# Performance work log

Measured on AMD Instinct MI355X. Metric: run time of the kernel, lower is better.

## Reference

```python
import jax, jax.numpy as jnp
import numpy as np

ALPHA = 1.0
K = 5          # kernel height == width
STRIDE = 1


def extract_patches(x, k, stride):
    """x: (N, C, H, W) -> (N, k*k*C, Ho, Wo), feature order (kh, kw, c)
    to match k.view(kh*kw*C, F) flattening of a (kh, kw, C, F) kernel."""
    p = jax.lax.conv_general_dilated_patches(x, (k, k), (stride, stride), 'VALID')
    N, _, Ho, Wo = p.shape
    C = x.shape[1]
    # conv_general_dilated_patches is channel-major: (C, kh, kw) -> reorder to (kh, kw, C)
    p = p.reshape(N, C, k, k, Ho, Wo).transpose(0, 2, 3, 1, 4, 5)
    return p.reshape(N, k * k * C, Ho, Wo)


def setup_inputs():
    key = jax.random.key(0)
    kx, kk1, kk2 = jax.random.split(key, 3)
    N, C, H, W = 8, 4, 64, 64
    F = 16
    # xavier-uniform-ish scale for kernels
    limit = float(np.sqrt(6.0 / (K * K * C + F)))
    x = jax.random.normal(kx, (N, C, H, W), jnp.float32)
    k1 = jax.random.uniform(kk1, (K, K, C, F), jnp.float32, -limit, limit)
    k2 = jax.random.uniform(kk2, (K, K, C, F), jnp.float32, -limit, limit)
    bias = jnp.zeros((F,), jnp.float32)
    return {"x": x, "k1": k1, "k2": k2, "bias": bias}


def _smooth_max(patches, kflat):
    # patches: (N, P, Ho, Wo); kflat: (P, F)
    z = patches[:, :, None] + kflat[None, :, :, None, None]  # (N, P, F, Ho, Wo)
    w = jax.nn.softmax(ALPHA * z, axis=1)  # exp(alpha*z)/sum over patch dim (stable)
    return jnp.sum(z * w, axis=1)          # (N, F, Ho, Wo)


def reference(x, k1, k2, bias):
    kh, kw, C, F = k1.shape
    patches = extract_patches(x, kh, STRIDE)        # (N, kh*kw*C, Ho, Wo)
    y11 = _smooth_max(patches, k1.reshape(-1, F))   # smooth-max of  x + k1
    y21 = _smooth_max(-patches, k2.reshape(-1, F))  # smooth-max of -x + k2
    return y11 + y21 + bias[None, :, None, None]
```

## Files before the change

kernel.cpp:

```cpp
#include <hip/hip_runtime.h>

#define NN 8
#define CC 4
#define HH 64
#define WW 64
#define KK 5
#define FF 16
#define HO 60
#define WO 60
#define PP (KK * KK * CC)


__global__ void smorph_weights(const float* __restrict__ k1,
                               const float* __restrict__ k2,
                               float4* __restrict__ wq) {
    int i = blockIdx.x * blockDim.x + threadIdx.x;
    if (i < PP * FF) {
        float a = k1[i], b = k2[i];
        float ea = __expf(a), eb = __expf(b);
        wq[i] = make_float4(ea, a * ea, eb, b * eb);
    }
}

__global__ __launch_bounds__(256) void smorph_conv(
        const float* __restrict__ x, const float4* __restrict__ wq,
        const float* __restrict__ bias, float* __restrict__ out) {
    __shared__ float4 pq[CC * KK * 64 + 4];

    int b = blockIdx.x;
    int n = b / HO;
    int ho = b % HO;
    int t = threadIdx.x;

    for (int i = t; i < CC * KK * 64; i += 256) {
        int w = i & 63;
        int cr = i >> 6;
        int c = cr / KK, r = cr - c * KK;
        float v = x[((n * CC + c) * HH + (ho + r)) * WW + w];
        float e1 = __expf(v), e2 = __expf(-v);
        pq[i] = make_float4(e1, v * e1, e2, -v * e2);
    }
    __syncthreads();

    int lane = t & 63;
    int fbase = __builtin_amdgcn_readfirstlane(t >> 6) * 4;

    float d1[4] = {0.f, 0.f, 0.f, 0.f}, n1[4] = {0.f, 0.f, 0.f, 0.f};
    float d2[4] = {0.f, 0.f, 0.f, 0.f}, n2[4] = {0.f, 0.f, 0.f, 0.f};

#pragma unroll 1
    for (int c = 0; c < CC; ++c) {
#pragma unroll
        for (int kh = 0; kh < KK; ++kh) {
            const float4* prow = &pq[(c * KK + kh) * 64 + lane];
#pragma unroll
            for (int kw = 0; kw < KK; ++kw) {
                float4 q = prow[kw];
                const float4* wp = wq + ((kh * KK + kw) * CC + c) * FF + fbase;
#pragma unroll
                for (int j = 0; j < 4; ++j) {
                    float4 ww = wp[j];
                    d1[j] = fmaf(q.x, ww.x, d1[j]);
                    n1[j] = fmaf(q.y, ww.x, n1[j]);
                    n1[j] = fmaf(q.x, ww.y, n1[j]);
                    d2[j] = fmaf(q.z, ww.z, d2[j]);
                    n2[j] = fmaf(q.w, ww.z, n2[j]);
                    n2[j] = fmaf(q.z, ww.w, n2[j]);
                }
            }
        }
    }

    if (lane < WO) {
#pragma unroll
        for (int j = 0; j < 4; ++j) {
            int f = fbase + j;
            out[((size_t)(n * FF + f) * HO + ho) * WO + lane] =
                n1[j] / d1[j] + n2[j] / d2[j] + bias[f];
        }
    }
}

extern "C" void kernel_launch(void* const* d_in, const int* in_sizes, int n_in,
                              void* d_out, int out_size, void* d_ws, size_t ws_size,
                              hipStream_t stream) {
    const float* x    = (const float*)d_in[0];
    const float* k1   = (const float*)d_in[1];
    const float* k2   = (const float*)d_in[2];
    const float* bias = (const float*)d_in[3];
    float* out = (float*)d_out;

    float4* wq = (float4*)d_ws;

    smorph_weights<<<(PP * FF + 255) / 256, 256, 0, stream>>>(k1, k2, wq);
    smorph_conv<<<480, 256, 0, stream>>>(x, wq, bias, out);
}
```

Measured before the change: 82.49 us.

## Fuse weight precompute into conv kernel, split channels across waves, pack FMAs

Removes the separate weight-exponentiation kernel and recomputes exp(k) weights per block into LDS, so the second launch and its dependency go away. The block grows to 512 threads, with two wave groups each covering half of the input channels, and a shared-memory reduction combines their partial sums. Accumulators use 2-wide float vectors so the compiler can emit packed FMAs. The cost is that every block redundantly recomputes 1600 weight exponentials, plus an extra barrier and LDS traffic for the reduction.

```diff
diff --git a/kernel.cpp b/kernel.cpp
--- a/kernel.cpp
+++ b/kernel.cpp
@@ -10,73 +10,97 @@
 #define WO 60
 #define PP (KK * KK * CC)
 
+typedef float v4f __attribute__((ext_vector_type(4)));
+typedef float v2f __attribute__((ext_vector_type(2)));
 
-__global__ void smorph_weights(const float* __restrict__ k1,
-                               const float* __restrict__ k2,
-                               float4* __restrict__ wq) {
-    int i = blockIdx.x * blockDim.x + threadIdx.x;
-    if (i < PP * FF) {
-        float a = k1[i], b = k2[i];
-        float ea = __expf(a), eb = __expf(b);
-        wq[i] = make_float4(ea, a * ea, eb, b * eb);
-    }
-}
-
-__global__ __launch_bounds__(256) void smorph_conv(
-        const float* __restrict__ x, const float4* __restrict__ wq,
-        const float* __restrict__ bias, float* __restrict__ out) {
-    __shared__ float4 pq[CC * KK * 64 + 4];
+__global__ __launch_bounds__(512) void smorph_fused(
+        const float* __restrict__ x, const float* __restrict__ k1,
+        const float* __restrict__ k2, const float* __restrict__ bias,
+        float* __restrict__ out) {
+    __shared__ v4f pq[CC * KK * 64 + 4];
+    __shared__ v4f wlds[PP * 16];
+    __shared__ v2f red[4 * 8 * 64];
 
     int b = blockIdx.x;
     int n = b / HO;
-    int ho = b % HO;
+    int ho = b - n * HO;
     int t = threadIdx.x;
 
-    for (int i = t; i < CC * KK * 64; i += 256) {
+    for (int i = t; i < PP * 16; i += 512) {
+        int p = i >> 4, rem = i & 15, side = rem >> 3, f2 = rem & 7;
+        const float* kp = side ? k2 : k1;
+        float ka = kp[p * FF + 2 * f2];
+        float kb = kp[p * FF + 2 * f2 + 1];
+        float ea = __expf(ka), eb = __expf(kb);
+        v4f wv = {ea, eb, ka * ea, kb * eb};
+        wlds[i] = wv;
+    }
+    for (int i = t; i < CC * KK * 64; i += 512) {
         int w = i & 63;
         int cr = i >> 6;
         int c = cr / KK, r = cr - c * KK;
         float v = x[((n * CC + c) * HH + (ho + r)) * WW + w];
         float e1 = __expf(v), e2 = __expf(-v);
-        pq[i] = make_float4(e1, v * e1, e2, -v * e2);
+        v4f qv = {e1, v * e1, e2, -v * e2};
+        pq[i] = qv;
     }
     __syncthreads();
 
     int lane = t & 63;
-    int fbase = __builtin_amdgcn_readfirstlane(t >> 6) * 4;
+    int wid = t >> 6;
+    int fg = wid & 3;
+    int ch = wid >> 2;
+    int fp2 = fg * 2;
 
-    float d1[4] = {0.f, 0.f, 0.f, 0.f}, n1[4] = {0.f, 0.f, 0.f, 0.f};
-    float d2[4] = {0.f, 0.f, 0.f, 0.f}, n2[4] = {0.f, 0.f, 0.f, 0.f};
+    v2f d1[2], n1[2], d2[2], n2[2];
+#pragma unroll
+    for (int jj = 0; jj < 2; ++jj) {
+        d1[jj] = 0.f; n1[jj] = 0.f; d2[jj] = 0.f; n2[jj] = 0.f;
+    }
 
 #pragma unroll 1
-    for (int c = 0; c < CC; ++c) {
+    for (int ci = 0; ci < 2; ++ci) {
+        int c = ch * 2 + ci;
 #pragma unroll
         for (int kh = 0; kh < KK; ++kh) {
-            const float4* prow = &pq[(c * KK + kh) * 64 + lane];
+            const v4f* prow = &pq[(c * KK + kh) * 64 + lane];
 #pragma unroll
             for (int kw = 0; kw < KK; ++kw) {
-                float4 q = prow[kw];
-                const float4* wp = wq + ((kh * KK + kw) * CC + c) * FF + fbase;
+                v4f q = prow[kw];
+                const v4f* wp = &wlds[((kh * KK + kw) * CC + c) * 16 + fp2];
 #pragma unroll
-                for (int j = 0; j < 4; ++j) {
-                    float4 ww = wp[j];
-                    d1[j] = fmaf(q.x, ww.x, d1[j]);
-                    n1[j] = fmaf(q.y, ww.x, n1[j]);
-                    n1[j] = fmaf(q.x, ww.y, n1[j]);
-                    d2[j] = fmaf(q.z, ww.z, d2[j]);
-                    n2[j] = fmaf(q.w, ww.z, n2[j]);
-                    n2[j] = fmaf(q.z, ww.w, n2[j]);
+                for (int jp = 0; jp < 2; ++jp) {
+                    v4f w1 = wp[jp];
+                    v4f w2 = wp[8 + jp];
+                    d1[jp] += q.xx * w1.xy;
+                    n1[jp] += q.yy * w1.xy + q.xx * w1.zw;
+                    d2[jp] += q.zz * w2.xy;
+                    n2[jp] += q.ww * w2.xy + q.zz * w2.zw;
                 }
             }
         }
     }
 
-    if (lane < WO) {
+    v2f* rr = &red[fg * 8 * 64 + lane];
+    if (ch) {
+        rr[0 * 64] = d1[0]; rr[1 * 64] = d1[1];
+        rr[2 * 64] = n1[0]; rr[3 * 64] = n1[1];
+        rr[4 * 64] = d2[0]; rr[5 * 64] = d2[1];
+        rr[6 * 64] = n2[0]; rr[7 * 64] = n2[1];
+    }
+    __syncthreads();
+    if (!ch && lane < WO) {
+        d1[0] += rr[0 * 64]; d1[1] += rr[1 * 64];
+        n1[0] += rr[2 * 64]; n1[1] += rr[3 * 64];
+        d2[0] += rr[4 * 64]; d2[1] += rr[5 * 64];
+        n2[0] += rr[6 * 64]; n2[1] += rr[7 * 64];
 #pragma unroll
-        for (int j = 0; j < 4; ++j) {
-            int f = fbase + j;
-            out[((size_t)(n * FF + f) * HO + ho) * WO + lane] =
-                n1[j] / d1[j] + n2[j] / d2[j] + bias[f];
+        for (int jp = 0; jp < 2; ++jp) {
+            v2f o = n1[jp] / d1[jp] + n2[jp] / d2[jp];
+            int f0 = fg * 4 + 2 * jp;
+            out[((size_t)(n * FF + f0) * HO + ho) * WO + lane] = o.x + bias[f0];
+            out[((size_t)(n * FF + f0 + 1) * HO + ho) * WO + lane] =
+                o.y + bias[f0 + 1];
         }
     }
 }
@@ -90,8 +114,5 @@
     const float* bias = (const float*)d_in[3];
     float* out = (float*)d_out;
 
-    float4* wq = (float4*)d_ws;
-
-    smorph_weights<<<(PP * FF + 255) / 256, 256, 0, stream>>>(k1, k2, wq);
-    smorph_conv<<<480, 256, 0, stream>>>(x, wq, bias, out);
+    smorph_fused<<<480, 512, 0, stream>>>(x, k1, k2, bias, out);
 }
```

New measurement: 70.82 us. 14.1% less time.

## Split channel reduction across waves and filter halves with LDS reduction

Applied to the files above, without the earlier changes.

Each block now handles half of the filters for one output row, with 8 waves of 512 threads. Each wave covers one input channel and a group of four filters. Partial sums from the four channel waves are combined through LDS before the division. Weights are reordered into a filter-group-major, structure-of-arrays layout so each wave reads them as scalar-friendly contiguous loads. The goal is more parallelism (960 blocks, four times the waves) and a shorter serial FMA chain per thread, paid for with duplicated exp work per block, an extra sync, and LDS reduction traffic.

```diff
diff --git a/kernel.cpp b/kernel.cpp
--- a/kernel.cpp
+++ b/kernel.cpp
@@ -10,73 +10,117 @@
 #define WO 60
 #define PP (KK * KK * CC)
 
+typedef float v4f __attribute__((ext_vector_type(4)));
+
+#define PQ_ELEMS (CC * KK * 64)
+#define LDS_TOT 1536
 
 __global__ void smorph_weights(const float* __restrict__ k1,
                                const float* __restrict__ k2,
-                               float4* __restrict__ wq) {
+                               float* __restrict__ wq) {
     int i = blockIdx.x * blockDim.x + threadIdx.x;
-    if (i < PP * FF) {
-        float a = k1[i], b = k2[i];
-        float ea = __expf(a), eb = __expf(b);
-        wq[i] = make_float4(ea, a * ea, eb, b * eb);
+    if (i < 4 * PP * 16) {
+        int idx16 = i >> 4;
+        int ff = idx16 / PP;
+        int p = idx16 - ff * PP;
+        int j = i & 15;
+        int grp = j >> 2;
+        int fi = j & 3;
+        int f = ff * 4 + fi;
+        const float* kp = (grp >> 1) ? k2 : k1;
+        float kv = kp[p * FF + f];
+        float e = __expf(kv);
+        wq[i] = (grp & 1) ? kv * e : e;
     }
 }
 
-__global__ __launch_bounds__(256) void smorph_conv(
-        const float* __restrict__ x, const float4* __restrict__ wq,
+__global__ __launch_bounds__(512) void smorph_conv(
+        const float* __restrict__ x, const float* __restrict__ wq,
         const float* __restrict__ bias, float* __restrict__ out) {
-    __shared__ float4 pq[CC * KK * 64 + 4];
+    __shared__ v4f lds[LDS_TOT];
+    v4f* pq = lds;
 
     int b = blockIdx.x;
-    int n = b / HO;
-    int ho = b % HO;
+    int n = b / (HO * 2);
+    int rem = b - n * (HO * 2);
+    int ho = rem >> 1;
+    int fgh = rem & 1;
     int t = threadIdx.x;
 
-    for (int i = t; i < CC * KK * 64; i += 256) {
+    for (int i = t; i < PQ_ELEMS; i += 512) {
         int w = i & 63;
         int cr = i >> 6;
         int c = cr / KK, r = cr - c * KK;
         float v = x[((n * CC + c) * HH + (ho + r)) * WW + w];
         float e1 = __expf(v), e2 = __expf(-v);
-        pq[i] = make_float4(e1, v * e1, e2, -v * e2);
+        pq[i] = (v4f){e1, v * e1, e2, -v * e2};
     }
     __syncthreads();
 
     int lane = t & 63;
-    int fbase = __builtin_amdgcn_readfirstlane(t >> 6) * 4;
+    int wid = t >> 6;
+    int cw = wid & 3;
+    int fgl = wid >> 2;
+
+    int wbi = __builtin_amdgcn_readfirstlane(((fgh * 2 + fgl) * PP + cw) * 16);
+    const float* wb = wq + wbi;
 
     float d1[4] = {0.f, 0.f, 0.f, 0.f}, n1[4] = {0.f, 0.f, 0.f, 0.f};
     float d2[4] = {0.f, 0.f, 0.f, 0.f}, n2[4] = {0.f, 0.f, 0.f, 0.f};
 
+    const v4f* pbase = pq + (cw * KK) * 64 + lane;
+
 #pragma unroll 1
-    for (int c = 0; c < CC; ++c) {
+    for (int kh = 0; kh < KK; ++kh) {
+        const v4f* prow = pbase + kh * 64;
+        v4f q[KK];
 #pragma unroll
-        for (int kh = 0; kh < KK; ++kh) {
-            const float4* prow = &pq[(c * KK + kh) * 64 + lane];
+        for (int kw = 0; kw < KK; ++kw) q[kw] = prow[kw];
 #pragma unroll
-            for (int kw = 0; kw < KK; ++kw) {
-                float4 q = prow[kw];
-                const float4* wp = wq + ((kh * KK + kw) * CC + c) * FF + fbase;
+        for (int kw = 0; kw < KK; ++kw) {
+            const float* wp = wb + (kh * KK + kw) * (CC * 16);
+            v4f qv = q[kw];
 #pragma unroll
-                for (int j = 0; j < 4; ++j) {
-                    float4 ww = wp[j];
-                    d1[j] = fmaf(q.x, ww.x, d1[j]);
-                    n1[j] = fmaf(q.y, ww.x, n1[j]);
-                    n1[j] = fmaf(q.x, ww.y, n1[j]);
-                    d2[j] = fmaf(q.z, ww.z, d2[j]);
-                    n2[j] = fmaf(q.w, ww.z, n2[j]);
-                    n2[j] = fmaf(q.z, ww.w, n2[j]);
-                }
+            for (int j = 0; j < 4; ++j) {
+                float ea1 = wp[j], ba1 = wp[4 + j];
+                float ea2 = wp[8 + j], bb2 = wp[12 + j];
+                d1[j] = fmaf(qv.x, ea1, d1[j]);
+                n1[j] = fmaf(qv.y, ea1, n1[j]);
+                n1[j] = fmaf(qv.x, ba1, n1[j]);
+                d2[j] = fmaf(qv.z, ea2, d2[j]);
+                n2[j] = fmaf(qv.w, ea2, n2[j]);
+                n2[j] = fmaf(qv.z, bb2, n2[j]);
             }
         }
     }
 
-    if (lane < WO) {
+    v4f* red = lds;
+    __syncthreads();
+    if (cw) {
+        v4f* rr = red + (((cw - 1) * 2 + fgl) * 4) * 64 + lane;
+        rr[0 * 64] = (v4f){d1[0], d1[1], d1[2], d1[3]};
+        rr[1 * 64] = (v4f){n1[0], n1[1], n1[2], n1[3]};
+        rr[2 * 64] = (v4f){d2[0], d2[1], d2[2], d2[3]};
+        rr[3 * 64] = (v4f){n2[0], n2[1], n2[2], n2[3]};
+    }
+    __syncthreads();
+    if (!cw && lane < WO) {
+#pragma unroll
+        for (int rcw = 0; rcw < 3; ++rcw) {
+            const v4f* rr = red + ((rcw * 2 + fgl) * 4) * 64 + lane;
+            v4f t0 = rr[0 * 64], t1 = rr[1 * 64];
+            v4f t2 = rr[2 * 64], t3 = rr[3 * 64];
+#pragma unroll
+            for (int j = 0; j < 4; ++j) {
+                d1[j] += t0[j]; n1[j] += t1[j];
+                d2[j] += t2[j]; n2[j] += t3[j];
+            }
+        }
+        int f0 = (fgh * 2 + fgl) * 4;
 #pragma unroll
         for (int j = 0; j < 4; ++j) {
-            int f = fbase + j;
-            out[((size_t)(n * FF + f) * HO + ho) * WO + lane] =
-                n1[j] / d1[j] + n2[j] / d2[j] + bias[f];
+            float o = n1[j] / d1[j] + n2[j] / d2[j] + bias[f0 + j];
+            out[((size_t)(n * FF + f0 + j) * HO + ho) * WO + lane] = o;
         }
     }
 }
@@ -89,9 +133,8 @@
     const float* k2   = (const float*)d_in[2];
     const float* bias = (const float*)d_in[3];
     float* out = (float*)d_out;
+    float* wq = (float*)d_ws;
 
-    float4* wq = (float4*)d_ws;
-
-    smorph_weights<<<(PP * FF + 255) / 256, 256, 0, stream>>>(k1, k2, wq);
-    smorph_conv<<<480, 256, 0, stream>>>(x, wq, bias, out);
+    smorph_weights<<<(4 * PP * 16 + 255) / 256, 256, 0, stream>>>(k1, k2, wq);
+    smorph_conv<<<NN * HO * 2, 512, 0, stream>>>(x, wq, bias, out);
 }
```

After: 70.90 us. 1.16x faster.
